# Performance work log

Hardware: AMD Instinct MI355X
Metric: run time of the kernel (lower is better)

## Reference

```python
import jax, jax.numpy as jnp
import numpy as np

B, S, E, H = 2, 2048, 1024, 16
D = E // H  # head_dim = 64
SCALE = float(np.sqrt(D))


def setup_inputs() -> dict:
    root = jax.random.key(0)
    ks = jax.random.split(root, 12)
    inp = {
        "query": jax.random.normal(ks[0], (B, S, E), dtype=jnp.float32),
        "key": jax.random.normal(ks[1], (B, S, E), dtype=jnp.float32),
        "value": jax.random.normal(ks[2], (B, S, E), dtype=jnp.float32),
        "mask": jax.random.randint(ks[3], (B, S, S), 0, 2, dtype=jnp.int32),
        # Linear weights stored torch-style as [out, in]; init scale ~ 1/sqrt(E)
        "Wq": jax.random.normal(ks[4], (E, E), dtype=jnp.float32) / np.sqrt(E),
        "bq": jnp.zeros((E,), dtype=jnp.float32),
        "Wk": jax.random.normal(ks[5], (E, E), dtype=jnp.float32) / np.sqrt(E),
        "bk": jnp.zeros((E,), dtype=jnp.float32),
        "Wv": jax.random.normal(ks[6], (E, E), dtype=jnp.float32) / np.sqrt(E),
        "bv": jnp.zeros((E,), dtype=jnp.float32),
        "Wo": jax.random.normal(ks[7], (E, E), dtype=jnp.float32) / np.sqrt(E),
        "bo": jnp.zeros((E,), dtype=jnp.float32),
    }
    return inp


def reference(query, key, value, mask, Wq, bq, Wk, bk, Wv, bv, Wo, bo):
    # Projections (torch Linear: x @ W.T + b)
    Q = query @ Wq.T + bq
    K = key @ Wk.T + bk
    V = value @ Wv.T + bv
    # [B, S, E] -> [B, H, S, D]
    Q = Q.reshape(B, S, H, D).transpose(0, 2, 1, 3)
    K = K.reshape(B, S, H, D).transpose(0, 2, 1, 3)
    V = V.reshape(B, S, H, D).transpose(0, 2, 1, 3)
    # Scaled dot-product scores [B, H, S, S]
    scores = jnp.einsum("bhqd,bhkd->bhqk", Q, K) / SCALE
    # mask==0 positions -> -1e9 (mask broadcast over heads)
    scores = jnp.where(mask[:, None, :, :] == 0, jnp.float32(-1e9), scores)
    attn = jax.nn.softmax(scores, axis=-1)  # dropout is identity in eval
    out = jnp.einsum("bhqk,bhkd->bhqd", attn, V)
    out = out.transpose(0, 2, 1, 3).reshape(B, S, E)
    output = out @ Wo.T + bo
    avg_attn = attn.mean(axis=1)  # [B, S, S]
    return output, avg_attn
```

## Files before the change

kernel.cpp:

```cpp
#include <hip/hip_runtime.h>
#include <stdint.h>

#define BB 2
#define SS 2048
#define EE 1024
#define HH 16
#define DD 64
#define C1 0.18033688f
#define NT (SS / 64)

typedef _Float16 h16;
typedef _Float16 f16x8 __attribute__((ext_vector_type(8)));
typedef _Float16 f16x4 __attribute__((ext_vector_type(4)));
typedef float f32x4 __attribute__((ext_vector_type(4)));

#define SWZ(row, j) ((j) ^ ((row) & 7))

__device__ __forceinline__ void async_ld16(const void* g, void* l) {
  __builtin_amdgcn_global_load_lds((__attribute__((address_space(1))) void*)g,
                                   (__attribute__((address_space(3))) void*)l,
                                   16, 0, 0);
}

__global__ __launch_bounds__(256) void cvt_qkv(const float* __restrict__ q,
                                               const float* __restrict__ k,
                                               const float* __restrict__ v,
                                               h16* __restrict__ oq, h16* __restrict__ ok,
                                               h16* __restrict__ ov, int n4) {
  const float* s;
  h16* d;
  if (blockIdx.y == 0) { s = q; d = oq; }
  else if (blockIdx.y == 1) { s = k; d = ok; }
  else { s = v; d = ov; }
  int i = blockIdx.x * 256 + threadIdx.x;
  if (i >= n4) return;
  const float4 t = reinterpret_cast<const float4*>(s)[i];
  f16x4 o = {(_Float16)t.x, (_Float16)t.y, (_Float16)t.z, (_Float16)t.w};
  *reinterpret_cast<f16x4*>(d + i * 4) = o;
}

__global__ __launch_bounds__(256) void cvt_w4(const float* __restrict__ w0, const float* __restrict__ w1,
                                              const float* __restrict__ w2, const float* __restrict__ w3,
                                              h16* __restrict__ o0, h16* __restrict__ o1,
                                              h16* __restrict__ o2, h16* __restrict__ o3, int n4) {
  const float* s;
  h16* d;
  if (blockIdx.y == 0) { s = w0; d = o0; }
  else if (blockIdx.y == 1) { s = w1; d = o1; }
  else if (blockIdx.y == 2) { s = w2; d = o2; }
  else { s = w3; d = o3; }
  int i = blockIdx.x * 256 + threadIdx.x;
  if (i >= n4) return;
  const float4 t = reinterpret_cast<const float4*>(s)[i];
  f16x4 o = {(_Float16)t.x, (_Float16)t.y, (_Float16)t.z, (_Float16)t.w};
  *reinterpret_cast<f16x4*>(d + i * 4) = o;
}

__global__ __launch_bounds__(256) void pack_mask(const int* __restrict__ mask,
                                                 unsigned long long* __restrict__ pk) {
  const size_t i = (size_t)blockIdx.x * 256 + threadIdx.x;
  const unsigned long long b = __ballot(mask[i] != 0);
  if ((threadIdx.x & 63) == 0) pk[i >> 6] = b;
}

template <int MODE>
__global__ __launch_bounds__(256, 2) void gemm_bt(const h16* __restrict__ A,
                                                  const h16* __restrict__ Bw,
                                                  const float* __restrict__ bias,
                                                  void* __restrict__ out) {
  constexpr int K = EE;
  __shared__ h16 As[2][128 * 64];
  __shared__ h16 Bs[2][64 * 64];
  const int tid = threadIdx.x;
  const int lane = tid & 63, w = tid >> 6;
  const int cg = lane & 15, rg = lane >> 4;
  const int wr = w >> 1, wc = w & 1;
  const int row0 = blockIdx.y * 128, col0 = blockIdx.x * 64;

  f32x4 acc[4][2] = {};

  const h16* Ag = A + (size_t)row0 * K;
  const h16* Bg = Bw + (size_t)col0 * K;

  auto stage = [&](int k0, int bi) {
#pragma unroll
    for (int i = 0; i < 4; ++i) {
      const int c = i * 256 + tid, row = c >> 3, jg = SWZ(row, c & 7);
      async_ld16(Ag + (size_t)row * K + k0 + jg * 8, (char*)As[bi] + (i * 256 + w * 64) * 16);
    }
#pragma unroll
    for (int i = 0; i < 2; ++i) {
      const int c = i * 256 + tid, row = c >> 3, jg = SWZ(row, c & 7);
      async_ld16(Bg + (size_t)row * K + k0 + jg * 8, (char*)Bs[bi] + (i * 256 + w * 64) * 16);
    }
  };

  stage(0, 0);
  __syncthreads();
  for (int ks = 0; ks < K / 64; ++ks) {
    const int cur = ks & 1;
    if (ks + 1 < K / 64) stage((ks + 1) * 64, cur ^ 1);
#pragma unroll
    for (int kk = 0; kk < 2; ++kk) {
      f16x8 af[4], bfr[2];
#pragma unroll
      for (int m = 0; m < 4; ++m) {
        const int row = wr * 64 + m * 16 + cg;
        af[m] = *(const f16x8*)&As[cur][row * 64 + SWZ(row, kk * 4 + rg) * 8];
      }
#pragma unroll
      for (int n = 0; n < 2; ++n) {
        const int row = wc * 32 + n * 16 + cg;
        bfr[n] = *(const f16x8*)&Bs[cur][row * 64 + SWZ(row, kk * 4 + rg) * 8];
      }
#pragma unroll
      for (int m = 0; m < 4; ++m)
#pragma unroll
        for (int n = 0; n < 2; ++n)
          acc[m][n] = __builtin_amdgcn_mfma_f32_16x16x32_f16(af[m], bfr[n], acc[m][n], 0, 0, 0);
    }
    __syncthreads();
  }

#pragma unroll
  for (int n = 0; n < 2; ++n) {
    const int col = col0 + wc * 32 + n * 16 + cg;
    const float bv = bias[col];
#pragma unroll
    for (int m = 0; m < 4; ++m) {
#pragma unroll
      for (int j = 0; j < 4; ++j) {
        const int row = row0 + wr * 64 + m * 16 + rg * 4 + j;
        const float v = acc[m][n][j] + bv;
        if (MODE == 2) {
          ((float*)out)[(size_t)row * EE + col] = v;
        } else {
          const int b = row >> 11, s = row & (SS - 1);
          const int h = col >> 6, d = col & (DD - 1);
          size_t idx;
          if (MODE == 0) idx = (((size_t)b * HH + h) * SS + s) * DD + d;
          else           idx = (((size_t)b * HH + h) * DD + d) * SS + s;
          ((h16*)out)[idx] = (_Float16)v;
        }
      }
    }
  }
}

__global__ __launch_bounds__(256, 2) void attn_fwd(
    const h16* __restrict__ Qh, const h16* __restrict__ Kh, const h16* __restrict__ Vt,
    const uint2* __restrict__ mpk, h16* __restrict__ O, float* __restrict__ Crow) {
  __shared__ h16 Ks[2][64 * 64];
  __shared__ h16 Vs[2][64 * 64];
  __shared__ h16 Ps[4][16][72];
  const int tid = threadIdx.x;
  const int lane = tid & 63, w = tid >> 6;
  const int cg = lane & 15, rg = lane >> 4;
  const int qt = blockIdx.x, bh = blockIdx.y;
  const int b = bh >> 4, h = bh & (HH - 1);
  const int q0 = qt * 64 + w * 16;

  const h16* Qbase = Qh + ((size_t)bh * SS + q0 + cg) * DD;
  const f16x8 qf0 = *(const f16x8*)(Qbase + rg * 8);
  const f16x8 qf1 = *(const f16x8*)(Qbase + 32 + rg * 8);

  f32x4 o[4] = {};
  float mrun[4] = {-INFINITY, -INFINITY, -INFINITY, -INFINITY};
  float lrun[4] = {0.f, 0.f, 0.f, 0.f};

  const h16* Kg = Kh + (size_t)bh * SS * DD;
  const h16* Vg = Vt + (size_t)bh * DD * SS;
  const uint2* mb = mpk + ((size_t)b * SS + q0) * NT;

  auto stage = [&](int k0, int bi) {
#pragma unroll
    for (int i = 0; i < 2; ++i) {
      const int c = i * 256 + tid, row = c >> 3, jg = SWZ(row, c & 7);
      async_ld16(Kg + (size_t)(k0 + row) * DD + jg * 8, (char*)Ks[bi] + (i * 256 + w * 64) * 16);
      async_ld16(Vg + (size_t)row * SS + k0 + jg * 8, (char*)Vs[bi] + (i * 256 + w * 64) * 16);
    }
  };

  stage(0, 0);
  __syncthreads();
  for (int kt = 0; kt < NT; ++kt) {
    const int cur = kt & 1;
    if (kt + 1 < NT) stage((kt + 1) * 64, cur ^ 1);

    uint2 pk[4];
#pragma unroll
    for (int j = 0; j < 4; ++j) pk[j] = mb[(rg * 4 + j) * NT + kt];

    f32x4 sc[4];
#pragma unroll
    for (int n = 0; n < 4; ++n) {
      const int row = n * 16 + cg;
      const f16x8 kf0 = *(const f16x8*)&Ks[cur][row * 64 + SWZ(row, rg) * 8];
      const f16x8 kf1 = *(const f16x8*)&Ks[cur][row * 64 + SWZ(row, rg + 4) * 8];
      f32x4 z = {};
      z = __builtin_amdgcn_mfma_f32_16x16x32_f16(qf0, kf0, z, 0, 0, 0);
      sc[n] = __builtin_amdgcn_mfma_f32_16x16x32_f16(qf1, kf1, z, 0, 0, 0);
    }

    float scl[4];
#pragma unroll
    for (int j = 0; j < 4; ++j) {
      const int r = rg * 4 + j;
      float v[4];
#pragma unroll
      for (int n = 0; n < 4; ++n) {
        const unsigned wbits = (n & 2) ? pk[j].y : pk[j].x;
        const bool on = (wbits >> ((n & 1) * 16 + cg)) & 1u;
        v[n] = on ? sc[n][j] * C1 : -1e9f;
      }
      float tm = fmaxf(fmaxf(v[0], v[1]), fmaxf(v[2], v[3]));
      tm = fmaxf(tm, __shfl_xor(tm, 1));
      tm = fmaxf(tm, __shfl_xor(tm, 2));
      tm = fmaxf(tm, __shfl_xor(tm, 4));
      tm = fmaxf(tm, __shfl_xor(tm, 8));
      const float mn = fmaxf(mrun[j], tm);
      scl[j] = exp2f(mrun[j] - mn);
      mrun[j] = mn;
      float ps = 0.f;
#pragma unroll
      for (int n = 0; n < 4; ++n) {
        const float p = exp2f(v[n] - mn);
        ps += p;
        Ps[w][r][n * 16 + cg] = (_Float16)p;
      }
      ps += __shfl_xor(ps, 1);
      ps += __shfl_xor(ps, 2);
      ps += __shfl_xor(ps, 4);
      ps += __shfl_xor(ps, 8);
      lrun[j] = lrun[j] * scl[j] + ps;
    }
#pragma unroll
    for (int n = 0; n < 4; ++n)
#pragma unroll
      for (int j = 0; j < 4; ++j) o[n][j] *= scl[j];

#pragma unroll
    for (int kkb = 0; kkb < 2; ++kkb) {
      const f16x8 pa = *(const f16x8*)&Ps[w][cg][kkb * 32 + rg * 8];
#pragma unroll
      for (int n = 0; n < 4; ++n) {
        const int row = n * 16 + cg;
        const f16x8 vf = *(const f16x8*)&Vs[cur][row * 64 + SWZ(row, kkb * 4 + rg) * 8];
        o[n] = __builtin_amdgcn_mfma_f32_16x16x32_f16(pa, vf, o[n], 0, 0, 0);
      }
    }
    __syncthreads();
  }

  float rl[4];
#pragma unroll
  for (int j = 0; j < 4; ++j) rl[j] = 1.f / lrun[j];
#pragma unroll
  for (int n = 0; n < 4; ++n)
#pragma unroll
    for (int j = 0; j < 4; ++j) {
      const int s = q0 + rg * 4 + j;
      O[((size_t)b * SS + s) * EE + h * DD + n * 16 + cg] = (_Float16)(o[n][j] * rl[j]);
    }
  if (cg == 0) {
#pragma unroll
    for (int j = 0; j < 4; ++j) {
      const int s = q0 + rg * 4 + j;
      Crow[(size_t)bh * SS + s] = mrun[j] + __log2f(lrun[j]);
    }
  }
}

__global__ __launch_bounds__(256, 2) void avg_attn_k(
    const h16* __restrict__ Qh, const h16* __restrict__ Kh,
    const uint2* __restrict__ mpk, const float* __restrict__ Crow,
    float* __restrict__ outAvg) {
  const int tid = threadIdx.x;
  const int lane = tid & 63, w = tid >> 6;
  const int cg = lane & 15, rg = lane >> 4;
  const int kt = blockIdx.x, qt = blockIdx.y, b = blockIdx.z;
  const int q0 = qt * 64 + w * 16, k0 = kt * 64;

  float mf[4][4];
#pragma unroll
  for (int j = 0; j < 4; ++j) {
    const uint2 pk = mpk[((size_t)b * SS + q0 + rg * 4 + j) * NT + kt];
#pragma unroll
    for (int n = 0; n < 4; ++n) {
      const unsigned wbits = (n & 2) ? pk.y : pk.x;
      mf[n][j] = ((wbits >> ((n & 1) * 16 + cg)) & 1u) ? 1.f : 0.f;
    }
  }

  f32x4 acc[4] = {};
#pragma unroll
  for (int h4 = 0; h4 < HH; h4 += 4) {
    f16x8 qf[4][2];
    float Cm[4][4];
#pragma unroll
    for (int hh = 0; hh < 4; ++hh) {
      const int bh = b * HH + h4 + hh;
      const h16* Qb = Qh + ((size_t)bh * SS + q0 + cg) * DD;
      qf[hh][0] = *(const f16x8*)(Qb + rg * 8);
      qf[hh][1] = *(const f16x8*)(Qb + 32 + rg * 8);
#pragma unroll
      for (int j = 0; j < 4; ++j)
        Cm[hh][j] = Crow[(size_t)bh * SS + q0 + rg * 4 + j];
    }
#pragma unroll
    for (int n = 0; n < 4; ++n) {
      f16x8 kf[4][2];
#pragma unroll
      for (int hh = 0; hh < 4; ++hh) {
        const h16* kr = Kh + (((size_t)(b * HH + h4 + hh) * SS) + k0 + n * 16 + cg) * DD + rg * 8;
        kf[hh][0] = *(const f16x8*)kr;
        kf[hh][1] = *(const f16x8*)(kr + 32);
      }
#pragma unroll
      for (int hh = 0; hh < 4; ++hh) {
        f32x4 z = {};
        z = __builtin_amdgcn_mfma_f32_16x16x32_f16(qf[hh][0], kf[hh][0], z, 0, 0, 0);
        const f32x4 sc = __builtin_amdgcn_mfma_f32_16x16x32_f16(qf[hh][1], kf[hh][1], z, 0, 0, 0);
#pragma unroll
        for (int j = 0; j < 4; ++j)
          acc[n][j] += exp2f(fmaf(sc[j], C1, -Cm[hh][j])) * mf[n][j];
      }
    }
  }
#pragma unroll
  for (int n = 0; n < 4; ++n)
#pragma unroll
    for (int j = 0; j < 4; ++j)
      outAvg[((size_t)b * SS + q0 + rg * 4 + j) * SS + k0 + n * 16 + cg] = acc[n][j] * 0.0625f;
}

extern "C" void kernel_launch(void* const* d_in, const int* in_sizes, int n_in,
                              void* d_out, int out_size, void* d_ws, size_t ws_size,
                              hipStream_t stream) {
  const float* query = (const float*)d_in[0];
  const float* key_  = (const float*)d_in[1];
  const float* value = (const float*)d_in[2];
  const int*   mask  = (const int*)d_in[3];
  const float* Wq = (const float*)d_in[4];
  const float* bq = (const float*)d_in[5];
  const float* Wk = (const float*)d_in[6];
  const float* bk = (const float*)d_in[7];
  const float* Wv = (const float*)d_in[8];
  const float* bv = (const float*)d_in[9];
  const float* Wo = (const float*)d_in[10];
  const float* bo = (const float*)d_in[11];

  const size_t SZ_SE = (size_t)BB * SS * EE;
  h16* qx  = (h16*)d_ws;
  h16* kx  = qx + SZ_SE;
  h16* vx  = kx + SZ_SE;
  h16* wqx = vx + SZ_SE;
  h16* wkx = wqx + EE * EE;
  h16* wvx = wkx + EE * EE;
  h16* wox = wvx + EE * EE;
  h16* Qd  = wox + EE * EE;
  h16* Kd  = Qd + SZ_SE;
  h16* Vtd = Kd + SZ_SE;
  h16* Od  = Vtd + SZ_SE;
  float* Cr = (float*)(Od + SZ_SE);
  unsigned long long* mpk = (unsigned long long*)(Cr + (size_t)BB * HH * SS);

  float* outp = (float*)d_out;
  float* avgp = outp + SZ_SE;

  pack_mask<<<(BB * SS * SS) / 256, 256, 0, stream>>>(mask, mpk);
  cvt_qkv<<<dim3(4096, 3), 256, 0, stream>>>(query, key_, value, qx, kx, vx, (int)(SZ_SE / 4));
  cvt_w4<<<dim3(1024, 4), 256, 0, stream>>>(Wq, Wk, Wv, Wo, wqx, wkx, wvx, wox, EE * EE / 4);

  gemm_bt<0><<<dim3(16, 32), 256, 0, stream>>>(qx, wqx, bq, Qd);
  gemm_bt<0><<<dim3(16, 32), 256, 0, stream>>>(kx, wkx, bk, Kd);
  gemm_bt<1><<<dim3(16, 32), 256, 0, stream>>>(vx, wvx, bv, Vtd);

  attn_fwd<<<dim3(SS / 64, BB * HH), 256, 0, stream>>>(Qd, Kd, Vtd, (const uint2*)mpk, Od, Cr);

  avg_attn_k<<<dim3(SS / 64, SS / 64, BB), 256, 0, stream>>>(Qd, Kd, (const uint2*)mpk, Cr, avgp);

  gemm_bt<2><<<dim3(16, 32), 256, 0, stream>>>(Od, wox, bo, outp);
}
```

Baseline: 525.1 us.

## Retile GEMMs, fold softmax scale into Q, lazy rescale, LDS-stage K in avg kernel

GEMM tiles shrink from 128x64 to 64x64 with more blocks and a higher occupancy hint, and the Q projection now pre-multiplies by the softmax log2 scale. The attention kernel goes to 512 threads covering 128 queries per block, so each staged K/V tile serves twice as many rows. It also skips the running-max rescale unless the max grows by more than 8, and applies the mask after exponentiation instead of substituting -1e9. The avg-attention kernel double-buffers each head's K tile through LDS instead of reading it directly from global per wave. Risks include fp16 overflow margin from deferred rescaling and fully-masked rows behaving differently from the reference's uniform -1e9 handling.

```diff
diff --git a/kernel.cpp b/kernel.cpp
--- a/kernel.cpp
+++ b/kernel.cpp
@@ -63,35 +63,31 @@
   if ((threadIdx.x & 63) == 0) pk[i >> 6] = b;
 }
 
-template <int MODE>
-__global__ __launch_bounds__(256, 2) void gemm_bt(const h16* __restrict__ A,
+template <int MODE, bool SCALEQ>
+__global__ __launch_bounds__(256, 4) void gemm_bt(const h16* __restrict__ A,
                                                   const h16* __restrict__ Bw,
                                                   const float* __restrict__ bias,
                                                   void* __restrict__ out) {
   constexpr int K = EE;
-  __shared__ h16 As[2][128 * 64];
+  __shared__ h16 As[2][64 * 64];
   __shared__ h16 Bs[2][64 * 64];
   const int tid = threadIdx.x;
   const int lane = tid & 63, w = tid >> 6;
   const int cg = lane & 15, rg = lane >> 4;
   const int wr = w >> 1, wc = w & 1;
-  const int row0 = blockIdx.y * 128, col0 = blockIdx.x * 64;
-
-  f32x4 acc[4][2] = {};
+  const int row0 = blockIdx.y * 64, col0 = blockIdx.x * 64;
+
+  f32x4 acc[2][2] = {};
 
   const h16* Ag = A + (size_t)row0 * K;
   const h16* Bg = Bw + (size_t)col0 * K;
 
   auto stage = [&](int k0, int bi) {
 #pragma unroll
-    for (int i = 0; i < 4; ++i) {
-      const int c = i * 256 + tid, row = c >> 3, jg = SWZ(row, c & 7);
-      async_ld16(Ag + (size_t)row * K + k0 + jg * 8, (char*)As[bi] + (i * 256 + w * 64) * 16);
-    }
-#pragma unroll
     for (int i = 0; i < 2; ++i) {
       const int c = i * 256 + tid, row = c >> 3, jg = SWZ(row, c & 7);
-      async_ld16(Bg + (size_t)row * K + k0 + jg * 8, (char*)Bs[bi] + (i * 256 + w * 64) * 16);
+      async_ld16(Ag + (size_t)row * K + k0 + jg * 8, (char*)As[bi] + c * 16);
+      async_ld16(Bg + (size_t)row * K + k0 + jg * 8, (char*)Bs[bi] + c * 16);
     }
   };
 
@@ -102,10 +98,10 @@
     if (ks + 1 < K / 64) stage((ks + 1) * 64, cur ^ 1);
 #pragma unroll
     for (int kk = 0; kk < 2; ++kk) {
-      f16x8 af[4], bfr[2];
-#pragma unroll
-      for (int m = 0; m < 4; ++m) {
-        const int row = wr * 64 + m * 16 + cg;
+      f16x8 af[2], bfr[2];
+#pragma unroll
+      for (int m = 0; m < 2; ++m) {
+        const int row = wr * 32 + m * 16 + cg;
         af[m] = *(const f16x8*)&As[cur][row * 64 + SWZ(row, kk * 4 + rg) * 8];
       }
 #pragma unroll
@@ -114,7 +110,7 @@
         bfr[n] = *(const f16x8*)&Bs[cur][row * 64 + SWZ(row, kk * 4 + rg) * 8];
       }
 #pragma unroll
-      for (int m = 0; m < 4; ++m)
+      for (int m = 0; m < 2; ++m)
 #pragma unroll
         for (int n = 0; n < 2; ++n)
           acc[m][n] = __builtin_amdgcn_mfma_f32_16x16x32_f16(af[m], bfr[n], acc[m][n], 0, 0, 0);
@@ -127,11 +123,12 @@
     const int col = col0 + wc * 32 + n * 16 + cg;
     const float bv = bias[col];
 #pragma unroll
-    for (int m = 0; m < 4; ++m) {
+    for (int m = 0; m < 2; ++m) {
 #pragma unroll
       for (int j = 0; j < 4; ++j) {
-        const int row = row0 + wr * 64 + m * 16 + rg * 4 + j;
-        const float v = acc[m][n][j] + bv;
+        const int row = row0 + wr * 32 + m * 16 + rg * 4 + j;
+        float v = acc[m][n][j] + bv;
+        if (SCALEQ) v *= C1;
         if (MODE == 2) {
           ((float*)out)[(size_t)row * EE + col] = v;
         } else {
@@ -147,18 +144,18 @@
   }
 }
 
-__global__ __launch_bounds__(256, 2) void attn_fwd(
+__global__ __launch_bounds__(512, 4) void attn_fwd(
     const h16* __restrict__ Qh, const h16* __restrict__ Kh, const h16* __restrict__ Vt,
     const uint2* __restrict__ mpk, h16* __restrict__ O, float* __restrict__ Crow) {
   __shared__ h16 Ks[2][64 * 64];
   __shared__ h16 Vs[2][64 * 64];
-  __shared__ h16 Ps[4][16][72];
+  __shared__ h16 Ps[8][16][72];
   const int tid = threadIdx.x;
   const int lane = tid & 63, w = tid >> 6;
   const int cg = lane & 15, rg = lane >> 4;
   const int qt = blockIdx.x, bh = blockIdx.y;
   const int b = bh >> 4, h = bh & (HH - 1);
-  const int q0 = qt * 64 + w * 16;
+  const int q0 = qt * 128 + w * 16;
 
   const h16* Qbase = Qh + ((size_t)bh * SS + q0 + cg) * DD;
   const f16x8 qf0 = *(const f16x8*)(Qbase + rg * 8);
@@ -173,12 +170,9 @@
   const uint2* mb = mpk + ((size_t)b * SS + q0) * NT;
 
   auto stage = [&](int k0, int bi) {
-#pragma unroll
-    for (int i = 0; i < 2; ++i) {
-      const int c = i * 256 + tid, row = c >> 3, jg = SWZ(row, c & 7);
-      async_ld16(Kg + (size_t)(k0 + row) * DD + jg * 8, (char*)Ks[bi] + (i * 256 + w * 64) * 16);
-      async_ld16(Vg + (size_t)row * SS + k0 + jg * 8, (char*)Vs[bi] + (i * 256 + w * 64) * 16);
-    }
+    const int row = tid >> 3, jg = SWZ(row, tid & 7);
+    async_ld16(Kg + (size_t)(k0 + row) * DD + jg * 8, (char*)Ks[bi] + tid * 16);
+    async_ld16(Vg + (size_t)row * SS + k0 + jg * 8, (char*)Vs[bi] + tid * 16);
   };
 
   stage(0, 0);
@@ -202,42 +196,46 @@
       sc[n] = __builtin_amdgcn_mfma_f32_16x16x32_f16(qf1, kf1, z, 0, 0, 0);
     }
 
-    float scl[4];
+    float tmv[4];
 #pragma unroll
     for (int j = 0; j < 4; ++j) {
-      const int r = rg * 4 + j;
-      float v[4];
+      float a = fmaxf(fmaxf(sc[0][j], sc[1][j]), fmaxf(sc[2][j], sc[3][j]));
+      a = fmaxf(a, __shfl_xor(a, 1));
+      a = fmaxf(a, __shfl_xor(a, 2));
+      a = fmaxf(a, __shfl_xor(a, 4));
+      a = fmaxf(a, __shfl_xor(a, 8));
+      tmv[j] = a;
+    }
+    const float need = fmaxf(fmaxf(tmv[0] - mrun[0], tmv[1] - mrun[1]),
+                             fmaxf(tmv[2] - mrun[2], tmv[3] - mrun[3]));
+    if (!__all(need <= 8.0f)) {
+#pragma unroll
+      for (int j = 0; j < 4; ++j) {
+        const float mn = fmaxf(mrun[j], tmv[j]);
+        const float scl = exp2f(mrun[j] - mn);
+        mrun[j] = mn;
+        lrun[j] *= scl;
+#pragma unroll
+        for (int n = 0; n < 4; ++n) o[n][j] *= scl;
+      }
+    }
+#pragma unroll
+    for (int j = 0; j < 4; ++j) {
+      float ps = 0.f;
 #pragma unroll
       for (int n = 0; n < 4; ++n) {
-        const unsigned wbits = (n & 2) ? pk[j].y : pk[j].x;
-        const bool on = (wbits >> ((n & 1) * 16 + cg)) & 1u;
-        v[n] = on ? sc[n][j] * C1 : -1e9f;
-      }
-      float tm = fmaxf(fmaxf(v[0], v[1]), fmaxf(v[2], v[3]));
-      tm = fmaxf(tm, __shfl_xor(tm, 1));
-      tm = fmaxf(tm, __shfl_xor(tm, 2));
-      tm = fmaxf(tm, __shfl_xor(tm, 4));
-      tm = fmaxf(tm, __shfl_xor(tm, 8));
-      const float mn = fmaxf(mrun[j], tm);
-      scl[j] = exp2f(mrun[j] - mn);
-      mrun[j] = mn;
-      float ps = 0.f;
-#pragma unroll
-      for (int n = 0; n < 4; ++n) {
-        const float p = exp2f(v[n] - mn);
+        float p = exp2f(sc[n][j] - mrun[j]);
+        const unsigned wb = (n & 2) ? pk[j].y : pk[j].x;
+        p = ((wb >> ((n & 1) * 16 + cg)) & 1u) ? p : 0.f;
         ps += p;
-        Ps[w][r][n * 16 + cg] = (_Float16)p;
+        Ps[w][rg * 4 + j][n * 16 + cg] = (_Float16)p;
       }
       ps += __shfl_xor(ps, 1);
       ps += __shfl_xor(ps, 2);
       ps += __shfl_xor(ps, 4);
       ps += __shfl_xor(ps, 8);
-      lrun[j] = lrun[j] * scl[j] + ps;
-    }
-#pragma unroll
-    for (int n = 0; n < 4; ++n)
-#pragma unroll
-      for (int j = 0; j < 4; ++j) o[n][j] *= scl[j];
+      lrun[j] += ps;
+    }
 
 #pragma unroll
     for (int kkb = 0; kkb < 2; ++kkb) {
@@ -271,10 +269,11 @@
   }
 }
 
-__global__ __launch_bounds__(256, 2) void avg_attn_k(
+__global__ __launch_bounds__(256, 4) void avg_attn_k(
     const h16* __restrict__ Qh, const h16* __restrict__ Kh,
     const uint2* __restrict__ mpk, const float* __restrict__ Crow,
     float* __restrict__ outAvg) {
+  __shared__ h16 Ks[2][64 * 64];
   const int tid = threadIdx.x;
   const int lane = tid & 63, w = tid >> 6;
   const int cg = lane & 15, rg = lane >> 4;
@@ -292,40 +291,58 @@
     }
   }
 
+  auto stageK = [&](int hh, int bi) {
+    const h16* Kg = Kh + (((size_t)(b * HH + hh) * SS) + k0) * DD;
+#pragma unroll
+    for (int i = 0; i < 2; ++i) {
+      const int c = i * 256 + tid, row = c >> 3, jg = SWZ(row, c & 7);
+      async_ld16(Kg + (size_t)row * DD + jg * 8, (char*)Ks[bi] + c * 16);
+    }
+  };
+
+  const h16* Qq = Qh + (((size_t)b * HH) * SS + q0 + cg) * DD;
+  const float* Cq = Crow + ((size_t)b * HH) * SS + q0;
+
+  stageK(0, 0);
+  f16x8 qc0 = *(const f16x8*)(Qq + rg * 8);
+  f16x8 qc1 = *(const f16x8*)(Qq + 32 + rg * 8);
+  float Cmc[4];
+#pragma unroll
+  for (int j = 0; j < 4; ++j) Cmc[j] = Cq[rg * 4 + j];
+  __syncthreads();
+
   f32x4 acc[4] = {};
-#pragma unroll
-  for (int h4 = 0; h4 < HH; h4 += 4) {
-    f16x8 qf[4][2];
-    float Cm[4][4];
-#pragma unroll
-    for (int hh = 0; hh < 4; ++hh) {
-      const int bh = b * HH + h4 + hh;
-      const h16* Qb = Qh + ((size_t)bh * SS + q0 + cg) * DD;
-      qf[hh][0] = *(const f16x8*)(Qb + rg * 8);
-      qf[hh][1] = *(const f16x8*)(Qb + 32 + rg * 8);
+  for (int h = 0; h < HH; ++h) {
+    const int cur = h & 1;
+    f16x8 qn0 = qc0, qn1 = qc1;
+    float Cmn[4];
+#pragma unroll
+    for (int j = 0; j < 4; ++j) Cmn[j] = Cmc[j];
+    if (h + 1 < HH) {
+      stageK(h + 1, cur ^ 1);
+      const h16* Qb = Qq + (size_t)(h + 1) * SS * DD;
+      qn0 = *(const f16x8*)(Qb + rg * 8);
+      qn1 = *(const f16x8*)(Qb + 32 + rg * 8);
+#pragma unroll
+      for (int j = 0; j < 4; ++j) Cmn[j] = Cq[(size_t)(h + 1) * SS + rg * 4 + j];
+    }
+#pragma unroll
+    for (int n = 0; n < 4; ++n) {
+      const int row = n * 16 + cg;
+      const f16x8 kf0 = *(const f16x8*)&Ks[cur][row * 64 + SWZ(row, rg) * 8];
+      const f16x8 kf1 = *(const f16x8*)&Ks[cur][row * 64 + SWZ(row, rg + 4) * 8];
+      f32x4 z = {};
+      z = __builtin_amdgcn_mfma_f32_16x16x32_f16(qc0, kf0, z, 0, 0, 0);
+      const f32x4 sc = __builtin_amdgcn_mfma_f32_16x16x32_f16(qc1, kf1, z, 0, 0, 0);
 #pragma unroll
       for (int j = 0; j < 4; ++j)
-        Cm[hh][j] = Crow[(size_t)bh * SS + q0 + rg * 4 + j];
-    }
-#pragma unroll
-    for (int n = 0; n < 4; ++n) {
-      f16x8 kf[4][2];
-#pragma unroll
-      for (int hh = 0; hh < 4; ++hh) {
-        const h16* kr = Kh + (((size_t)(b * HH + h4 + hh) * SS) + k0 + n * 16 + cg) * DD + rg * 8;
-        kf[hh][0] = *(const f16x8*)kr;
-        kf[hh][1] = *(const f16x8*)(kr + 32);
-      }
-#pragma unroll
-      for (int hh = 0; hh < 4; ++hh) {
-        f32x4 z = {};
-        z = __builtin_amdgcn_mfma_f32_16x16x32_f16(qf[hh][0], kf[hh][0], z, 0, 0, 0);
-        const f32x4 sc = __builtin_amdgcn_mfma_f32_16x16x32_f16(qf[hh][1], kf[hh][1], z, 0, 0, 0);
-#pragma unroll
-        for (int j = 0; j < 4; ++j)
-          acc[n][j] += exp2f(fmaf(sc[j], C1, -Cm[hh][j])) * mf[n][j];
-      }
-    }
+        acc[n][j] = fmaf(exp2f(sc[j] - Cmc[j]), mf[n][j], acc[n][j]);
+    }
+    __syncthreads();
+    qc0 = qn0;
+    qc1 = qn1;
+#pragma unroll
+    for (int j = 0; j < 4; ++j) Cmc[j] = Cmn[j];
   }
 #pragma unroll
   for (int n = 0; n < 4; ++n)
@@ -372,13 +389,13 @@
   cvt_qkv<<<dim3(4096, 3), 256, 0, stream>>>(query, key_, value, qx, kx, vx, (int)(SZ_SE / 4));
   cvt_w4<<<dim3(1024, 4), 256, 0, stream>>>(Wq, Wk, Wv, Wo, wqx, wkx, wvx, wox, EE * EE / 4);
 
-  gemm_bt<0><<<dim3(16, 32), 256, 0, stream>>>(qx, wqx, bq, Qd);
-  gemm_bt<0><<<dim3(16, 32), 256, 0, stream>>>(kx, wkx, bk, Kd);
-  gemm_bt<1><<<dim3(16, 32), 256, 0, stream>>>(vx, wvx, bv, Vtd);
-
-  attn_fwd<<<dim3(SS / 64, BB * HH), 256, 0, stream>>>(Qd, Kd, Vtd, (const uint2*)mpk, Od, Cr);
+  gemm_bt<0, true ><<<dim3(16, 64), 256, 0, stream>>>(qx, wqx, bq, Qd);
+  gemm_bt<0, false><<<dim3(16, 64), 256, 0, stream>>>(kx, wkx, bk, Kd);
+  gemm_bt<1, false><<<dim3(16, 64), 256, 0, stream>>>(vx, wvx, bv, Vtd);
+
+  attn_fwd<<<dim3(SS / 128, BB * HH), 512, 0, stream>>>(Qd, Kd, Vtd, (const uint2*)mpk, Od, Cr);
 
   avg_attn_k<<<dim3(SS / 64, SS / 64, BB), 256, 0, stream>>>(Qd, Kd, (const uint2*)mpk, Cr, avgp);
 
-  gemm_bt<2><<<dim3(16, 32), 256, 0, stream>>>(Od, wox, bo, outp);
-}
+  gemm_bt<2, false><<<dim3(16, 64), 256, 0, stream>>>(Od, wox, bo, outp);
+}
```

Result: slower. 744.6 us (+41.8%).
